# Optimization experiments

Hardware: AMD Instinct MI355X
Metric: run time of the kernel (lower is better)

The kernel has to match this reference:

```python
import jax, jax.numpy as jnp
import numpy as np

N_NODES = 100000
N_EDGES = 1600000
IN_CH = 64
HIDDEN = 64
OUT_DIM = HIDDEN // 2  # 32


def setup_inputs() -> dict:
    key = jax.random.key(0)
    ks = jax.random.split(key, 10)
    x = jax.random.normal(ks[0], (N_NODES, IN_CH), dtype=jnp.float32)
    edge_index = jax.random.randint(ks[1], (2, N_EDGES), 0, N_NODES, dtype=jnp.int64)
    s = 1.0 / np.sqrt(IN_CH)
    sh = 1.0 / np.sqrt(HIDDEN)
    # SAGEConv layer 1: lin_l (with bias) on aggregated neighbors, lin_r (no bias) on root
    w1l = jax.random.uniform(ks[2], (HIDDEN, IN_CH), jnp.float32, -s, s)
    b1 = jax.random.uniform(ks[3], (HIDDEN,), jnp.float32, -s, s)
    w1r = jax.random.uniform(ks[4], (HIDDEN, IN_CH), jnp.float32, -s, s)
    # SAGEConv layer 2
    w2l = jax.random.uniform(ks[5], (HIDDEN, HIDDEN), jnp.float32, -sh, sh)
    b2 = jax.random.uniform(ks[6], (HIDDEN,), jnp.float32, -sh, sh)
    w2r = jax.random.uniform(ks[7], (HIDDEN, HIDDEN), jnp.float32, -sh, sh)
    # readout head
    wh = jax.random.uniform(ks[8], (OUT_DIM, HIDDEN), jnp.float32, -sh, sh)
    bh = jax.random.uniform(ks[9], (OUT_DIM,), jnp.float32, -sh, sh)
    return {"x": x, "edge_index": edge_index, "w1l": w1l, "b1": b1, "w1r": w1r,
            "w2l": w2l, "b2": b2, "w2r": w2r, "wh": wh, "bh": bh}


def _sage_conv(h, src, dst, wl, bl, wr):
    # mean-aggregate messages from src nodes onto dst nodes
    msg = h[src]                                            # [E, d]
    agg = jax.ops.segment_sum(msg, dst, num_segments=N_NODES)  # [N, d]
    deg = jax.ops.segment_sum(jnp.ones((msg.shape[0],), h.dtype), dst,
                              num_segments=N_NODES)            # [N]
    mean = agg / jnp.maximum(deg, 1.0)[:, None]
    return mean @ wl.T + bl + h @ wr.T


def reference(x, edge_index, w1l, b1, w1r, w2l, b2, w2r, wh, bh):
    src, dst = edge_index[0], edge_index[1]
    # dropout layers are identity in eval mode
    h = jax.nn.relu(_sage_conv(x, src, dst, w1l, b1, w1r))
    h = jax.nn.relu(_sage_conv(h, src, dst, w2l, b2, w2r))
    return h @ wh.T + bh
```

## Files before the change

kernel.cpp:

```cpp
#include <hip/hip_runtime.h>


#define D 64
#define OUTD 32
#define REG_SHIFT 8
#define REG_SIZE 256
#define BCHUNK 4096
#define PADQ 8
#define CAP 5120
#define OUTCAP 8960

#define OFF_FLAG     0
#define OFF_RCUR     64
#define OFF_DEG      576
#define OFF_ROWSTART 100928
#define OFF_INV      201280
#define OFF_COL      301632
#define OFF_EBUF     3804992
#define OFF_XB       5806912
#define OFF_H1B      9006944
#define OFF_WC1      15406976
#define OFF_WC2      15411072
#define OFF_WHB      15415168

typedef __attribute__((ext_vector_type(8))) short bf16x8;
typedef __attribute__((ext_vector_type(4))) float f32x4;
typedef __attribute__((ext_vector_type(2))) float f32x2;

__device__ __forceinline__ unsigned short bf16rne(float x) {
    unsigned u = __float_as_uint(x);
    unsigned r = (u + 0x7FFFu + ((u >> 16) & 1u)) >> 16;
    return (unsigned short)r;
}

__global__ void detect_init(const int* __restrict__ e32, int* __restrict__ flag,
                            int* __restrict__ rcur, int NR) {
    int t = threadIdx.x;
    if (t < 64) {
        int v = e32[2 * t + 1];
        unsigned long long m = __ballot(v != 0);
        if (t == 0) flag[0] = (m == 0ULL) ? 1 : 0;
    }
    if (t < NR) rcur[t] = t * CAP;
}

__global__ __launch_bounds__(256) void bin_prep(
        const int* __restrict__ e32, const int* __restrict__ flag,
        int* __restrict__ rcur, int* __restrict__ ebuf, int E, int NR, int bblocks,
        const float* __restrict__ x, unsigned short* __restrict__ xb,
        unsigned short* __restrict__ h1b,
        const float* __restrict__ w1l, const float* __restrict__ w1r,
        const float* __restrict__ w2l, const float* __restrict__ w2r,
        const float* __restrict__ wh,
        unsigned short* __restrict__ wcat1, unsigned short* __restrict__ wcat2,
        unsigned short* __restrict__ whb, int n4, int N) {
    __shared__ int stage[BCHUNK];
    __shared__ unsigned short rgn[BCHUNK];
    __shared__ int hist[512], lbase[512], startr[512], s1[512];
    int t = threadIdx.x;

    if (blockIdx.x >= bblocks) {
        int i = (blockIdx.x - bblocks) * 256 + t;
        if (i < n4) {
            float4 v = ((const float4*)x)[i];
            unsigned lo = (unsigned)bf16rne(v.x) | ((unsigned)bf16rne(v.y) << 16);
            unsigned hi = (unsigned)bf16rne(v.z) | ((unsigned)bf16rne(v.w) << 16);
            ((uint2*)xb)[i] = make_uint2(lo, hi);
            return;
        }
        int j = i - n4;
        if (j < 16) {
            ((uint2*)xb)[(size_t)N * 16 + j] = make_uint2(0u, 0u);
        } else if (j < 32) {
            ((uint2*)h1b)[(size_t)N * 16 + (j - 16)] = make_uint2(0u, 0u);
        } else if (j < 32 + 8192) {
            int q = j - 32;
            int o = q >> 7, k = q & 127;
            wcat1[q] = bf16rne(k < 64 ? w1l[o * 64 + k] : w1r[o * 64 + k - 64]);
        } else if (j < 32 + 16384) {
            int q = j - 32 - 8192;
            int o = q >> 7, k = q & 127;
            wcat2[q] = bf16rne(k < 64 ? w2l[o * 64 + k] : w2r[o * 64 + k - 64]);
        } else if (j < 32 + 16384 + 2048) {
            int q = j - 32 - 16384;
            whb[q] = bf16rne(wh[q]);
        }
        return;
    }

    int mode = flag[0];
    int base = blockIdx.x * BCHUNK;
    for (int i = t; i < 512; i += 256) hist[i] = 0;
    __syncthreads();
    for (int j = t; j < BCHUNK; j += 256) {
        int i = base + j;
        if (i < E) {
            int d = mode ? e32[2 * (E + i)] : e32[E + i];
            atomicAdd(&hist[d >> REG_SHIFT], 1);
        }
    }
    __syncthreads();
    {
        int* a = lbase; int* b = s1;
        for (int i = t; i < 512; i += 256) a[i] = hist[i];
        __syncthreads();
        for (int off = 1; off < 512; off <<= 1) {
            for (int i = t; i < 512; i += 256)
                b[i] = a[i] + ((i >= off) ? a[i - off] : 0);
            __syncthreads();
            int* tmp = a; a = b; b = tmp;
        }
        for (int i = t; i < 512; i += 256) {
            int incl = a[i];
            int ex = incl - hist[i];
            __syncthreads();
            lbase[i] = ex;
        }
        __syncthreads();
    }
    for (int i = t; i < 512; i += 256) {
        int st = 0;
        if (i < NR && hist[i] > 0) {
            st = atomicAdd(&rcur[i], hist[i]);
            int lim = (i + 1) * CAP - hist[i];
            if (st > lim) st = lim;
        }
        startr[i] = st;
    }
    __syncthreads();
    for (int i = t; i < 512; i += 256) hist[i] = 0;
    __syncthreads();
    for (int j = t; j < BCHUNK; j += 256) {
        int i = base + j;
        if (i < E) {
            int s = mode ? e32[2 * i]       : e32[i];
            int d = mode ? e32[2 * (E + i)] : e32[E + i];
            int r = d >> REG_SHIFT;
            int o = atomicAdd(&hist[r], 1);
            int pos = lbase[r] + o;
            stage[pos] = ((d & (REG_SIZE - 1)) << 24) | s;
            rgn[pos] = (unsigned short)r;
        }
    }
    __syncthreads();
    int count = E - base; if (count > BCHUNK) count = BCHUNK;
    for (int i = t; i < count; i += 256) {
        int r = rgn[i];
        ebuf[startr[r] + (i - lbase[r])] = stage[i];
    }
}

__global__ __launch_bounds__(256) void build_csr(
        const int* __restrict__ ebuf, const int* __restrict__ rcur,
        int* __restrict__ degP, int* __restrict__ rowStartP, float* __restrict__ inv,
        int* __restrict__ colP, int N) {
    __shared__ int hist[REG_SIZE], cur[REG_SIZE], sA[REG_SIZE], sB[REG_SIZE];
    int r = blockIdx.x;
    int t = threadIdx.x;
    int lo = r << REG_SHIFT;
    int e0 = r * CAP, e1 = rcur[r];
    int colPbase = r * OUTCAP;
    hist[t] = 0;
    __syncthreads();
    for (int i = e0 + t; i < e1; i += 256)
        atomicAdd(&hist[((unsigned)ebuf[i]) >> 24], 1);
    __syncthreads();
    int v = hist[t];
    int vp = (v + PADQ - 1) & ~(PADQ - 1);
    int* a = sA; int* b = sB;
    a[t] = vp;
    __syncthreads();
    for (int off = 1; off < 256; off <<= 1) {
        b[t] = a[t] + ((t >= off) ? a[t - off] : 0);
        __syncthreads();
        int* tmp = a; a = b; b = tmp;
    }
    int startP = colPbase + (a[t] - vp);
    int node = lo + t;
    if (node < N) {
        degP[node] = vp;
        rowStartP[node] = startP;
        inv[node] = 1.0f / (float)(v > 0 ? v : 1);
    }
    cur[t] = startP;
    __syncthreads();
    for (int i = e0 + t; i < e1; i += 256) {
        int p = ebuf[i];
        int pos = atomicAdd(&cur[((unsigned)p) >> 24], 1);
        colP[pos] = (p & 0xFFFFFF) << 7;
    }
    __syncthreads();
    int zoff = N << 7;
    for (int k = startP + v; k < startP + vp; ++k) colP[k] = zoff;
}

template <bool HEAD>
__global__ __launch_bounds__(256, 8) void fused_layer(
        const unsigned short* __restrict__ hb,
        const int* __restrict__ rowStartP, const int* __restrict__ degPv,
        const int* __restrict__ colP, const float* __restrict__ invdeg,
        const unsigned short* __restrict__ wcat,
        const float* __restrict__ bias,
        unsigned short* __restrict__ houtb,
        const unsigned short* __restrict__ whb,
        const float* __restrict__ bh,
        float* __restrict__ outp,
        int n) {
    __shared__ unsigned meanT[16 * 32];
    __shared__ unsigned short hT[HEAD ? 16 * 64 : 64];

    const int lane = threadIdx.x & 63;
    const int w    = threadIdx.x >> 6;
    const int half = lane >> 5, l31 = lane & 31;
    const int l15  = lane & 15, kg  = lane >> 4;
    const char* hbC = (const char*)hb;
    unsigned voff = (unsigned)(l31 << 2);

    const int nb = blockIdx.x * 16;

    for (int q = 0; q < 4; ++q) {
        int node = nb + w * 4 + q;
        int nodeC = node < n ? node : n - 1;
        nodeC = __builtin_amdgcn_readfirstlane(nodeC);
        int rs = rowStartP[nodeC];
        int dgp = degPv[nodeC];

        f32x2 a0 = {0.f, 0.f}, a1 = {0.f, 0.f}, a2 = {0.f, 0.f}, a3 = {0.f, 0.f};
        f32x2 a4 = {0.f, 0.f}, a5 = {0.f, 0.f}, a6 = {0.f, 0.f}, a7 = {0.f, 0.f};

        for (int base = 0; base < dgp; base += 64) {
            int cv = colP[rs + base + lane];
            int m = dgp - base; if (m > 64) m = 64;
            int pairs = m >> 1;
            int pb = half;
            int p = 0;
            for (; p + 8 <= pairs; p += 8) {
#define G(j, A) { \
                int cb = __shfl(cv, pb + 2 * (j)); \
                unsigned u = *(const unsigned*)(hbC + ((unsigned)cb + voff)); \
                f32x2 ww = {__uint_as_float(u << 16), __uint_as_float(u & 0xFFFF0000u)}; \
                A += ww; }
                G(0, a0)  G(1, a1)  G(2, a2)  G(3, a3)
                G(4, a4)  G(5, a5)  G(6, a6)  G(7, a7)
                pb += 16;
            }
            if (pairs & 4) {
                G(0, a0)  G(1, a1)  G(2, a2)  G(3, a3)
            }
#undef G
        }
        f32x2 s = ((a0 + a1) + (a2 + a3)) + ((a4 + a5) + (a6 + a7));
        float s0 = s.x + __shfl_xor(s.x, 32);
        float s1 = s.y + __shfl_xor(s.y, 32);
        float iv = invdeg[nodeC];
        if (!half) {
            int local = w * 4 + q;
            unsigned mo = (unsigned)bf16rne(s0 * iv) | ((unsigned)bf16rne(s1 * iv) << 16);
            int cb = l31 >> 2;
            meanT[local * 32 + ((cb ^ (local & 7)) << 2) + (l31 & 3)] = mo;
        }
    }
    __syncthreads();

    const int nt = w;
    bf16x8 Am[2];
#pragma unroll
    for (int s = 0; s < 2; ++s) {
        int cb = s * 4 + kg;
        Am[s] = *(const bf16x8*)&meanT[l15 * 32 + ((cb ^ (l15 & 7)) << 2)];
    }
    int arow = nb + l15; if (arow >= n) arow = n - 1;
    const unsigned short* orow = hb + (size_t)arow * 64 + kg * 8;
    bf16x8 Ao0 = *(const bf16x8*)(orow);
    bf16x8 Ao1 = *(const bf16x8*)(orow + 32);
    const unsigned short* wrow = wcat + (nt * 16 + l15) * 128 + kg * 8;
    bf16x8 B0 = *(const bf16x8*)(wrow);
    bf16x8 B1 = *(const bf16x8*)(wrow + 32);
    bf16x8 B2 = *(const bf16x8*)(wrow + 64);
    bf16x8 B3 = *(const bf16x8*)(wrow + 96);

    float bc = bias[nt * 16 + l15];
    f32x4 a = {bc, bc, bc, bc};
    a = __builtin_amdgcn_mfma_f32_16x16x32_bf16(Am[0], B0, a, 0, 0, 0);
    a = __builtin_amdgcn_mfma_f32_16x16x32_bf16(Am[1], B1, a, 0, 0, 0);
    a = __builtin_amdgcn_mfma_f32_16x16x32_bf16(Ao0,  B2, a, 0, 0, 0);
    a = __builtin_amdgcn_mfma_f32_16x16x32_bf16(Ao1,  B3, a, 0, 0, 0);

    if constexpr (!HEAD) {
#pragma unroll
        for (int r = 0; r < 4; ++r) {
            int rw = nb + kg * 4 + r;
            float h = fmaxf(a[r], 0.0f);
            if (rw < n) houtb[(size_t)rw * 64 + nt * 16 + l15] = bf16rne(h);
        }
    } else {
        int bGlob = nt * 2 + (l15 >> 3);
        int n7 = l15 & 7;
#pragma unroll
        for (int r = 0; r < 4; ++r) {
            int m = kg * 4 + r;
            float h = fmaxf(a[r], 0.0f);
            hT[m * 64 + ((bGlob ^ (m & 7)) * 8) + n7] = bf16rne(h);
        }
        __syncthreads();
        if (w < 2) {
            bf16x8 hA[2];
#pragma unroll
            for (int s = 0; s < 2; ++s) {
                int kb = s * 4 + kg;
                hA[s] = *(const bf16x8*)(hT + l15 * 64 + ((kb ^ (l15 & 7)) * 8));
            }
            const unsigned short* hrow = whb + (w * 16 + l15) * 64 + kg * 8;
            bf16x8 H0 = *(const bf16x8*)(hrow);
            bf16x8 H1 = *(const bf16x8*)(hrow + 32);
            float bc2 = bh[w * 16 + l15];
            f32x4 a2 = {bc2, bc2, bc2, bc2};
            a2 = __builtin_amdgcn_mfma_f32_16x16x32_bf16(hA[0], H0, a2, 0, 0, 0);
            a2 = __builtin_amdgcn_mfma_f32_16x16x32_bf16(hA[1], H1, a2, 0, 0, 0);
#pragma unroll
            for (int r = 0; r < 4; ++r) {
                int rw = nb + kg * 4 + r;
                if (rw < n) outp[(size_t)rw * 32 + w * 16 + l15] = a2[r];
            }
        }
    }
}

extern "C" void kernel_launch(void* const* d_in, const int* in_sizes, int n_in,
                              void* d_out, int out_size, void* d_ws, size_t ws_size,
                              hipStream_t stream) {
    const float* x   = (const float*)d_in[0];
    const int* edges = (const int*)d_in[1];
    const float* w1l = (const float*)d_in[2];
    const float* b1  = (const float*)d_in[3];
    const float* w1r = (const float*)d_in[4];
    const float* w2l = (const float*)d_in[5];
    const float* b2  = (const float*)d_in[6];
    const float* w2r = (const float*)d_in[7];
    const float* wh  = (const float*)d_in[8];
    const float* bh  = (const float*)d_in[9];
    float* out = (float*)d_out;

    const int N = in_sizes[0] / D;
    const int E = in_sizes[1] / 2;
    const int NR = (N + REG_SIZE - 1) >> REG_SHIFT;

    int* ws = (int*)d_ws;
    int*            flag     = ws + OFF_FLAG;
    int*            rcur     = ws + OFF_RCUR;
    int*            degP     = ws + OFF_DEG;
    int*            rowStartP= ws + OFF_ROWSTART;
    float*          inv      = (float*)(ws + OFF_INV);
    int*            colP     = ws + OFF_COL;
    int*            ebuf     = ws + OFF_EBUF;
    unsigned short* xb       = (unsigned short*)(ws + OFF_XB);
    unsigned short* h1b      = (unsigned short*)(ws + OFF_H1B);
    unsigned short* wcat1    = (unsigned short*)(ws + OFF_WC1);
    unsigned short* wcat2    = (unsigned short*)(ws + OFF_WC2);
    unsigned short* whb      = (unsigned short*)(ws + OFF_WHB);

    detect_init<<<1, 512, 0, stream>>>(edges, flag, rcur, NR);
    int bblocks = (E + BCHUNK - 1) / BCHUNK;
    int n4 = N * D / 4;
    int pblocks = (n4 + 32 + 16384 + 2048 + 255) / 256;
    bin_prep<<<bblocks + pblocks, 256, 0, stream>>>(
        edges, flag, rcur, ebuf, E, NR, bblocks,
        x, xb, h1b, w1l, w1r, w2l, w2r, wh, wcat1, wcat2, whb, n4, N);
    build_csr<<<NR, 256, 0, stream>>>(ebuf, rcur, degP, rowStartP, inv, colP, N);

    int ntiles = (N + 15) / 16;

    fused_layer<false><<<ntiles, 256, 0, stream>>>(
        xb, rowStartP, degP, colP, inv, wcat1, b1,
        h1b, nullptr, nullptr, nullptr, N);
    fused_layer<true><<<ntiles, 256, 0, stream>>>(
        h1b, rowStartP, degP, colP, inv, wcat2, b2,
        nullptr, whb, bh, out, N);
}
```

Baseline: 137.4 us.

## Drop detect_init kernel and widen gather to 8-byte loads per lane

The separate detect_init launch is removed. The index-width detection now happens inside each bin_prep block through a syncthreads_or, and the region cursors are zeroed with a memset and stored as relative offsets. The gather in fused_layer now has each group of 16 lanes load 8 bytes (4 bf16) per neighbor row, covering four neighbors per instruction instead of two with 4-byte loads. This halves the number of load instructions and shuffles per edge, at the cost of an extra cross-lane reduction stage and more redundant detection reads across blocks.

```diff
diff --git a/kernel.cpp b/kernel.cpp
--- a/kernel.cpp
+++ b/kernel.cpp
@@ -10,7 +10,6 @@
 #define CAP 5120
 #define OUTCAP 8960
 
-#define OFF_FLAG     0
 #define OFF_RCUR     64
 #define OFF_DEG      576
 #define OFF_ROWSTART 100928
@@ -33,19 +32,8 @@
     return (unsigned short)r;
 }
 
-__global__ void detect_init(const int* __restrict__ e32, int* __restrict__ flag,
-                            int* __restrict__ rcur, int NR) {
-    int t = threadIdx.x;
-    if (t < 64) {
-        int v = e32[2 * t + 1];
-        unsigned long long m = __ballot(v != 0);
-        if (t == 0) flag[0] = (m == 0ULL) ? 1 : 0;
-    }
-    if (t < NR) rcur[t] = t * CAP;
-}
-
 __global__ __launch_bounds__(256) void bin_prep(
-        const int* __restrict__ e32, const int* __restrict__ flag,
+        const int* __restrict__ e32,
         int* __restrict__ rcur, int* __restrict__ ebuf, int E, int NR, int bblocks,
         const float* __restrict__ x, unsigned short* __restrict__ xb,
         unsigned short* __restrict__ h1b,
@@ -88,7 +76,9 @@
         return;
     }
 
-    int mode = flag[0];
+    int vflag = (t < 64) ? (e32[2 * t + 1] != 0) : 0;
+    int mode = __syncthreads_or(vflag) ? 0 : 1;
+
     int base = blockIdx.x * BCHUNK;
     for (int i = t; i < 512; i += 256) hist[i] = 0;
     __syncthreads();
@@ -121,7 +111,7 @@
     for (int i = t; i < 512; i += 256) {
         int st = 0;
         if (i < NR && hist[i] > 0) {
-            st = atomicAdd(&rcur[i], hist[i]);
+            st = i * CAP + atomicAdd(&rcur[i], hist[i]);
             int lim = (i + 1) * CAP - hist[i];
             if (st > lim) st = lim;
         }
@@ -158,7 +148,7 @@
     int r = blockIdx.x;
     int t = threadIdx.x;
     int lo = r << REG_SHIFT;
-    int e0 = r * CAP, e1 = rcur[r];
+    int e0 = r * CAP, e1 = r * CAP + rcur[r];
     int colPbase = r * OUTCAP;
     hist[t] = 0;
     __syncthreads();
@@ -211,12 +201,18 @@
 
     const int lane = threadIdx.x & 63;
     const int w    = threadIdx.x >> 6;
-    const int half = lane >> 5, l31 = lane & 31;
-    const int l15  = lane & 15, kg  = lane >> 4;
+    const int qw   = lane >> 4, l15 = lane & 15;
+    const int kg   = lane >> 4;
     const char* hbC = (const char*)hb;
-    unsigned voff = (unsigned)(l31 << 2);
+    unsigned o8 = (unsigned)(l15 << 3);
 
     const int nb = blockIdx.x * 16;
+
+#define LOF(u) __uint_as_float((u) << 16)
+#define HIF(u) __uint_as_float((u) & 0xFFFF0000u)
+#define ACC(u, AX, AY) { \
+    f32x2 wx = {LOF((u).x), HIF((u).x)}; AX += wx; \
+    f32x2 wy = {LOF((u).y), HIF((u).y)}; AY += wy; }
 
     for (int q = 0; q < 4; ++q) {
         int node = nb + w * 4 + q;
@@ -225,41 +221,77 @@
         int rs = rowStartP[nodeC];
         int dgp = degPv[nodeC];
 
-        f32x2 a0 = {0.f, 0.f}, a1 = {0.f, 0.f}, a2 = {0.f, 0.f}, a3 = {0.f, 0.f};
-        f32x2 a4 = {0.f, 0.f}, a5 = {0.f, 0.f}, a6 = {0.f, 0.f}, a7 = {0.f, 0.f};
+        f32x2 aX0 = {0.f, 0.f}, aX1 = {0.f, 0.f}, aX2 = {0.f, 0.f}, aX3 = {0.f, 0.f};
+        f32x2 aY0 = {0.f, 0.f}, aY1 = {0.f, 0.f}, aY2 = {0.f, 0.f}, aY3 = {0.f, 0.f};
 
         for (int base = 0; base < dgp; base += 64) {
             int cv = colP[rs + base + lane];
             int m = dgp - base; if (m > 64) m = 64;
-            int pairs = m >> 1;
-            int pb = half;
             int p = 0;
-            for (; p + 8 <= pairs; p += 8) {
-#define G(j, A) { \
-                int cb = __shfl(cv, pb + 2 * (j)); \
-                unsigned u = *(const unsigned*)(hbC + ((unsigned)cb + voff)); \
-                f32x2 ww = {__uint_as_float(u << 16), __uint_as_float(u & 0xFFFF0000u)}; \
-                A += ww; }
-                G(0, a0)  G(1, a1)  G(2, a2)  G(3, a3)
-                G(4, a4)  G(5, a5)  G(6, a6)  G(7, a7)
-                pb += 16;
+            for (; p + 32 <= m; p += 32) {
+                int c0 = __shfl(cv, p + qw);
+                int c1 = __shfl(cv, p + 4 + qw);
+                int c2 = __shfl(cv, p + 8 + qw);
+                int c3 = __shfl(cv, p + 12 + qw);
+                int c4 = __shfl(cv, p + 16 + qw);
+                int c5 = __shfl(cv, p + 20 + qw);
+                int c6 = __shfl(cv, p + 24 + qw);
+                int c7 = __shfl(cv, p + 28 + qw);
+                uint2 u0 = *(const uint2*)(hbC + ((unsigned)c0 + o8));
+                uint2 u1 = *(const uint2*)(hbC + ((unsigned)c1 + o8));
+                uint2 u2 = *(const uint2*)(hbC + ((unsigned)c2 + o8));
+                uint2 u3 = *(const uint2*)(hbC + ((unsigned)c3 + o8));
+                uint2 u4 = *(const uint2*)(hbC + ((unsigned)c4 + o8));
+                uint2 u5 = *(const uint2*)(hbC + ((unsigned)c5 + o8));
+                uint2 u6 = *(const uint2*)(hbC + ((unsigned)c6 + o8));
+                uint2 u7 = *(const uint2*)(hbC + ((unsigned)c7 + o8));
+                ACC(u0, aX0, aY0)  ACC(u1, aX1, aY1)
+                ACC(u2, aX2, aY2)  ACC(u3, aX3, aY3)
+                ACC(u4, aX0, aY0)  ACC(u5, aX1, aY1)
+                ACC(u6, aX2, aY2)  ACC(u7, aX3, aY3)
             }
-            if (pairs & 4) {
-                G(0, a0)  G(1, a1)  G(2, a2)  G(3, a3)
+            if (m & 16) {
+                int c0 = __shfl(cv, p + qw);
+                int c1 = __shfl(cv, p + 4 + qw);
+                int c2 = __shfl(cv, p + 8 + qw);
+                int c3 = __shfl(cv, p + 12 + qw);
+                uint2 u0 = *(const uint2*)(hbC + ((unsigned)c0 + o8));
+                uint2 u1 = *(const uint2*)(hbC + ((unsigned)c1 + o8));
+                uint2 u2 = *(const uint2*)(hbC + ((unsigned)c2 + o8));
+                uint2 u3 = *(const uint2*)(hbC + ((unsigned)c3 + o8));
+                ACC(u0, aX0, aY0)  ACC(u1, aX1, aY1)
+                ACC(u2, aX2, aY2)  ACC(u3, aX3, aY3)
+                p += 16;
             }
-#undef G
-        }
-        f32x2 s = ((a0 + a1) + (a2 + a3)) + ((a4 + a5) + (a6 + a7));
-        float s0 = s.x + __shfl_xor(s.x, 32);
-        float s1 = s.y + __shfl_xor(s.y, 32);
+            if (m & 8) {
+                int c0 = __shfl(cv, p + qw);
+                int c1 = __shfl(cv, p + 4 + qw);
+                uint2 u0 = *(const uint2*)(hbC + ((unsigned)c0 + o8));
+                uint2 u1 = *(const uint2*)(hbC + ((unsigned)c1 + o8));
+                ACC(u0, aX0, aY0)  ACC(u1, aX1, aY1)
+            }
+        }
+        f32x2 sX = (aX0 + aX1) + (aX2 + aX3);
+        f32x2 sY = (aY0 + aY1) + (aY2 + aY3);
+        sX.x += __shfl_xor(sX.x, 16);  sX.x += __shfl_xor(sX.x, 32);
+        sX.y += __shfl_xor(sX.y, 16);  sX.y += __shfl_xor(sX.y, 32);
+        sY.x += __shfl_xor(sY.x, 16);  sY.x += __shfl_xor(sY.x, 32);
+        sY.y += __shfl_xor(sY.y, 16);  sY.y += __shfl_xor(sY.y, 32);
         float iv = invdeg[nodeC];
-        if (!half) {
+        if (lane < 16) {
             int local = w * 4 + q;
-            unsigned mo = (unsigned)bf16rne(s0 * iv) | ((unsigned)bf16rne(s1 * iv) << 16);
-            int cb = l31 >> 2;
-            meanT[local * 32 + ((cb ^ (local & 7)) << 2) + (l31 & 3)] = mo;
-        }
-    }
+            unsigned m0 = (unsigned)bf16rne(sX.x * iv) | ((unsigned)bf16rne(sX.y * iv) << 16);
+            unsigned m1 = (unsigned)bf16rne(sY.x * iv) | ((unsigned)bf16rne(sY.y * iv) << 16);
+            int cidx = 2 * l15;
+            int cb = cidx >> 2;
+            int idx = ((cb ^ (local & 7)) << 2) + (cidx & 3);
+            meanT[local * 32 + idx]     = m0;
+            meanT[local * 32 + idx + 1] = m1;
+        }
+    }
+#undef ACC
+#undef LOF
+#undef HIF
     __syncthreads();
 
     const int nt = w;
@@ -346,7 +378,6 @@
     const int NR = (N + REG_SIZE - 1) >> REG_SHIFT;
 
     int* ws = (int*)d_ws;
-    int*            flag     = ws + OFF_FLAG;
     int*            rcur     = ws + OFF_RCUR;
     int*            degP     = ws + OFF_DEG;
     int*            rowStartP= ws + OFF_ROWSTART;
@@ -359,12 +390,12 @@
     unsigned short* wcat2    = (unsigned short*)(ws + OFF_WC2);
     unsigned short* whb      = (unsigned short*)(ws + OFF_WHB);
 
-    detect_init<<<1, 512, 0, stream>>>(edges, flag, rcur, NR);
+    hipMemsetAsync(rcur, 0, 512 * sizeof(int), stream);
     int bblocks = (E + BCHUNK - 1) / BCHUNK;
     int n4 = N * D / 4;
     int pblocks = (n4 + 32 + 16384 + 2048 + 255) / 256;
     bin_prep<<<bblocks + pblocks, 256, 0, stream>>>(
-        edges, flag, rcur, ebuf, E, NR, bblocks,
+        edges, rcur, ebuf, E, NR, bblocks,
         x, xb, h1b, w1l, w1r, w2l, w2r, wh, wcat1, wcat2, whb, n4, N);
     build_csr<<<NR, 256, 0, stream>>>(ebuf, rcur, degP, rowStartP, inv, colP, N);
 
```

After: 141.5 us. 2.9% more time.
